# Optimization experiments

Hardware: AMD Instinct MI355X
Metric: run time of the kernel (lower is better)

## Reference

```python
import jax, jax.numpy as jnp
import numpy as np
from jax import lax

# Module config (mirrors init_kwargs)
N, CIN, COUT, H, W = 16, 512, 512, 64, 64
KS = 3          # conv kernel_size
FACTOR = 2
GAIN = 1.0
LRMUL = 1.0
FIR_1D = np.array([1.0, 3.0, 3.0, 1.0], dtype=np.float32)

# upfirdn pad amounts as in the torch code
FIRN = 4
P = FIRN - FACTOR + (KS - 1)      # = 4
PAD0 = (P + 1) // 2               # = 2
PAD1 = P // 2                     # = 2
W_LRMUL = GAIN / np.sqrt(CIN * COUT * KS * KS)  # he_std * lrmul (use_wscale)
B_LRMUL = LRMUL
SQRT2 = np.float32(np.sqrt(2.0))


def setup_inputs() -> dict:
    key = jax.random.key(0)
    kx, kw, kb = jax.random.split(key, 3)
    x = jax.random.normal(kx, (N, CIN, H, W), dtype=jnp.float32)
    # weight init: randn * init_std, init_std = 1/lrmul = 1.0 under use_wscale
    weight = jax.random.normal(kw, (COUT, CIN, KS, KS), dtype=jnp.float32)
    bias = jax.random.normal(kb, (COUT,), dtype=jnp.float32) * 0.1
    kf = np.outer(FIR_1D, FIR_1D)
    kf = kf / kf.sum() * GAIN
    fir = jnp.asarray(kf, dtype=jnp.float32)  # [4,4], non-trainable
    return {"x": x, "weight": weight, "bias": bias, "fir": fir}


def _blur_and_resize(x, fir):
    # x: [N, C, H, W]; FIR blur via depthwise trick: fold C into batch.
    n, c, h, w = x.shape
    y = x.reshape(n * c, 1, h, w)
    y = jnp.pad(y, ((0, 0), (0, 0), (PAD0, PAD1), (PAD0, PAD1)))
    # valid conv with 4x4 FIR -> [n*c, 1, h+1, w+1]
    y = lax.conv_general_dilated(
        y, fir[None, None, :, :], window_strides=(1, 1), padding="VALID",
        dimension_numbers=("NCHW", "OIHW", "NCHW"))
    # F.interpolate(mode='nearest') from (h+1, w+1) back to (h, w):
    # torch nearest uses src = floor(dst * in/out) == (dst*(h+1))//h
    ri = (jnp.arange(h) * (h + 1)) // h
    ci = (jnp.arange(w) * (w + 1)) // w
    y = y[:, :, ri, :][:, :, :, ci]
    return y.reshape(n, c, h, w)


def reference(x, weight, bias, fir):
    y = _blur_and_resize(x, fir)
    # strided conv: stride=factor, padding=ks//2 (SAME-ish), cross-correlation
    out = lax.conv_general_dilated(
        y, weight * W_LRMUL, window_strides=(FACTOR, FACTOR),
        padding=[(KS // 2, KS // 2), (KS // 2, KS // 2)],
        dimension_numbers=("NCHW", "OIHW", "NCHW"))
    out = out + (bias * B_LRMUL)[None, :, None, None]
    out = jnp.where(out >= 0, out, 0.2 * out) * SQRT2  # leaky_relu(0.2) * sqrt(2)
    return out
```

## Files before the change

### kernel.cpp

```cpp
#include <hip/hip_runtime.h>
#include <hip/hip_bf16.h>
#include <stdint.h>

#define N_IMG 16
#define C_IN  512
#define C_OUT 512
#define H_IN  64
#define W_IN  64
#define OH    32
#define OW    32
#define PIX   (N_IMG*OH*OW)

#define YPH 65
#define YPW 33

#define W2_ELEMS (9*C_OUT*C_IN)
#define W2_BYTES (W2_ELEMS*2)

typedef __attribute__((ext_vector_type(8))) __bf16 bf16x8;
typedef __attribute__((ext_vector_type(4))) float  f32x4;

__device__ inline void gload_lds16(const void* g, void* l) {
  __builtin_amdgcn_global_load_lds(
      (const __attribute__((address_space(1))) void*)g,
      (__attribute__((address_space(3))) void*)l, 16, 0, 0);
}

__global__ __launch_bounds__(256) void prep_w_kernel(const float* __restrict__ w,
                                                     __hip_bfloat16* __restrict__ w2) {
  int id = blockIdx.x * 256 + threadIdx.x;
  const float* p = w + (size_t)id * 9;
  float v[9];
#pragma unroll
  for (int t = 0; t < 9; ++t) v[t] = p[t] * (1.0f/1536.0f);
#pragma unroll
  for (int t = 0; t < 9; ++t)
    w2[(size_t)t*(C_OUT*C_IN) + id] = __float2bfloat16(v[t]);
}

__global__ __launch_bounds__(256) void blur_kernel(const float* __restrict__ x,
                                                   __hip_bfloat16* __restrict__ yt) {
  __shared__ float obuf[2][32][65];
  const int tid = threadIdx.x;
  const int c   = tid >> 3;
  const int p8  = tid & 7;
  const int w8  = p8 * 8;
  const int r0  = blockIdx.x * 8;
  const int cib = blockIdx.y;
  const int n   = blockIdx.z;
  const float* xc = x + ((size_t)(n*C_IN + cib*32 + c) * H_IN) * W_IN + w8;

  {
    const uint4 z4 = {0u, 0u, 0u, 0u};
    if (tid < 16) {
      int hh  = r0 + (tid >> 1);
      int par = tid & 1;
      size_t slot = (((size_t)n*YPH + hh + 1)*2 + par)*YPW;
      uint4* p = (uint4*)(yt + slot*C_IN + cib*32);
      p[0]=z4; p[1]=z4; p[2]=z4; p[3]=z4;
    }
    if (blockIdx.x == 0 && tid < 66) {
      int par = tid / 33;
      int cc  = tid - par*33;
      size_t slot = ((size_t)n*YPH*2 + par)*YPW + cc;
      uint4* p = (uint4*)(yt + slot*C_IN + cib*32);
      p[0]=z4; p[1]=z4; p[2]=z4; p[3]=z4;
    }
  }

  const int rp_oc  = tid & 3;
  const int rp_p   = tid >> 2;
  const int rp_par = rp_p & 1;
  const int rp_ch  = rp_p >> 1;

  float cur[8], nxt[8];
  float h1[8], h2[8], h3[8];
#pragma unroll
  for (int j = 0; j < 8; ++j) { h1[j] = 0.f; h2[j] = 0.f; h3[j] = 0.f; }

  auto load_row = [&](int r, float* dst) {
    if (r >= 0 && r < H_IN) {
      const float4 a = *(const float4*)(xc + (size_t)r * W_IN);
      const float4 b = *(const float4*)(xc + (size_t)r * W_IN + 4);
      dst[0]=a.x; dst[1]=a.y; dst[2]=a.z; dst[3]=a.w;
      dst[4]=b.x; dst[5]=b.y; dst[6]=b.z; dst[7]=b.w;
    } else {
#pragma unroll
      for (int j = 0; j < 8; ++j) dst[j] = 0.f;
    }
  };

  load_row(r0 - 2, cur);
  for (int ri = 0; ri < 11; ++ri) {
    const int r = r0 - 2 + ri;
    if (ri < 10) load_row(r + 1, nxt);

    float l2 = __shfl_up(cur[6], 1);
    float l1 = __shfl_up(cur[7], 1);
    float rr = __shfl_down(cur[0], 1);
    if (p8 == 0) { l2 = 0.f; l1 = 0.f; }
    if (p8 == 7) { rr = 0.f; }
    float hc[8];
    hc[0] = l2 + 3.f*(l1 + cur[0]) + cur[1];
    hc[1] = l1 + 3.f*(cur[0] + cur[1]) + cur[2];
#pragma unroll
    for (int j = 2; j < 7; ++j) hc[j] = cur[j-2] + 3.f*(cur[j-1] + cur[j]) + cur[j+1];
    hc[7] = cur[5] + 3.f*(cur[6] + cur[7]) + rr;

    if (ri >= 3) {
      const int h = r - 1;
      const int b = ri & 1;
#pragma unroll
      for (int j = 0; j < 8; ++j)
        obuf[b][c][w8 + j] = (h3[j] + 3.f*(h2[j] + h1[j]) + hc[j]) * (1.0f/64.0f);
      __syncthreads();
      alignas(16) __hip_bfloat16 t16[8];
#pragma unroll
      for (int j = 0; j < 8; ++j)
        t16[j] = __float2bfloat16(obuf[b][rp_oc*8 + j][rp_p]);
      size_t slot = ((size_t)(n*YPH + h + 1)*2 + rp_par)*YPW + rp_ch + 1;
      *(uint4*)(yt + slot*C_IN + cib*32 + rp_oc*8) = *(uint4*)t16;
    }

#pragma unroll
    for (int j = 0; j < 8; ++j) {
      h3[j] = h2[j]; h2[j] = h1[j]; h1[j] = hc[j]; cur[j] = nxt[j];
    }
  }
}

#define ABYTES (128*64*2)
__global__ __launch_bounds__(256, 2) void conv_kernel(const __hip_bfloat16* __restrict__ w2,
                            const __hip_bfloat16* __restrict__ yt,
                            const float* __restrict__ bias,
                            float* __restrict__ out) {
  __shared__ __hip_bfloat16 Alds[2][128*64];
  __shared__ __hip_bfloat16 Blds[2][128*64];
  const int tid  = threadIdx.x;
  const int lane = tid & 63;
  const int wv   = tid >> 6;
  const int wm   = wv & 1;
  const int wn   = wv >> 1;
  const int cob0 = blockIdx.y * 128;
  const int pixb = blockIdx.x * 128;
  const int quad = lane >> 4;
  const int wvb  = tid & 192;

  size_t aoff[4];
  int    bseg8[4], bn65[4], boh2[4], bow_[4];
  int    ldsOff[4];
#pragma unroll
  for (int i = 0; i < 4; ++i) {
    int s = i*256 + tid;
    int r = s >> 3;
    int pp = s & 7;
    int gg = pp ^ (r & 7);
    aoff[i] = (size_t)(cob0 + r)*C_IN + gg*8;
    int gp = pixb + r;
    bn65[i] = (gp >> 10) * YPH;
    boh2[i] = ((gp >> 5) & 31) * 2;
    bow_[i] = gp & 31;
    bseg8[i] = gg*8;
    ldsOff[i] = (i*256 + wvb)*16;
  }

  auto stage = [&](int c, int b) {
    const int t   = c >> 3;
    const int cib = (c & 7) << 6;
    const int kh  = (t * 11) >> 5;
    const int kw  = t - kh*3;
    const int par = (kw == 1) ? 0 : 1;
    const int d   = (kw == 0) ? 0 : 1;
    const __hip_bfloat16* wt = w2 + (size_t)t * (C_OUT*C_IN) + cib;
#pragma unroll
    for (int i = 0; i < 4; ++i)
      gload_lds16(wt + aoff[i], (char*)Alds + b*ABYTES + ldsOff[i]);
#pragma unroll
    for (int i = 0; i < 4; ++i) {
      size_t slot = ((size_t)(bn65[i] + boh2[i] + kh)*2 + par)*YPW + bow_[i] + d;
      gload_lds16(yt + slot*C_IN + bseg8[i] + cib, (char*)Blds + b*ABYTES + ldsOff[i]);
    }
  };

  f32x4 acc[4][4];
  const f32x4 zero = {0.f, 0.f, 0.f, 0.f};
#pragma unroll
  for (int mi = 0; mi < 4; ++mi)
#pragma unroll
    for (int ni = 0; ni < 4; ++ni) acc[mi][ni] = zero;

  stage(0, 0);
#pragma unroll 2
  for (int cch = 0; cch < 72; ++cch) {
    __syncthreads();
    if (cch < 71) stage(cch + 1, (cch + 1) & 1);
    const int b = cch & 1;
    const char* Ab = (const char*)Alds + b*ABYTES;
    const char* Bb = (const char*)Blds + b*ABYTES;
#pragma unroll
    for (int kk = 0; kk < 2; ++kk) {
      bf16x8 af[4], bfr[4];
#pragma unroll
      for (int mi = 0; mi < 4; ++mi) {
        int r = wm*64 + mi*16 + (lane & 15);
        int gsg = kk*4 + quad;
        af[mi] = *(const bf16x8*)(Ab + r*128 + ((gsg ^ (r & 7))*16));
      }
#pragma unroll
      for (int ni = 0; ni < 4; ++ni) {
        int r = wn*64 + ni*16 + (lane & 15);
        int gsg = kk*4 + quad;
        bfr[ni] = *(const bf16x8*)(Bb + r*128 + ((gsg ^ (r & 7))*16));
      }
#pragma unroll
      for (int mi = 0; mi < 4; ++mi)
#pragma unroll
        for (int ni = 0; ni < 4; ++ni)
          acc[mi][ni] = __builtin_amdgcn_mfma_f32_16x16x32_bf16(af[mi], bfr[ni], acc[mi][ni], 0, 0, 0);
    }
  }

#pragma unroll
  for (int mi = 0; mi < 4; ++mi) {
#pragma unroll
    for (int reg = 0; reg < 4; ++reg) {
      int co = cob0 + wm*64 + mi*16 + quad*4 + reg;
      float bv = bias[co];
#pragma unroll
      for (int ni = 0; ni < 4; ++ni) {
        int gp  = pixb + wn*64 + ni*16 + (lane & 15);
        int n   = gp >> 10;
        int ohw = gp & 1023;
        float v = acc[mi][ni][reg] + bv;
        v = (v >= 0.f ? v : 0.2f*v) * 1.41421356f;
        out[(((size_t)n*C_OUT + co) << 10) + ohw] = v;
      }
    }
  }
}

extern "C" void kernel_launch(void* const* d_in, const int* in_sizes, int n_in,
                              void* d_out, int out_size, void* d_ws, size_t ws_size,
                              hipStream_t stream) {
  const float* x    = (const float*)d_in[0];
  const float* w    = (const float*)d_in[1];
  const float* bias = (const float*)d_in[2];
  float* out = (float*)d_out;
  __hip_bfloat16* w2 = (__hip_bfloat16*)d_ws;
  __hip_bfloat16* yt = (__hip_bfloat16*)((char*)d_ws + W2_BYTES);

  prep_w_kernel<<<(C_OUT*C_IN)/256, 256, 0, stream>>>(w, w2);
  blur_kernel<<<dim3(8, 16, 16), 256, 0, stream>>>(x, yt);
  conv_kernel<<<dim3(PIX/128, C_OUT/128), 256, 0, stream>>>(w2, yt, bias, out);
}
```

Baseline: 307.6 us.

## Load weight fragments directly from global into registers, drop A LDS staging

The weight (A) operand is no longer staged through shared memory. Each lane now loads its own MFMA fragments straight from global memory into a double-buffered register array, prefetched one K-chunk ahead. This halves LDS traffic and footprint and removes the LDS reads for A. In exchange it adds register pressure (32 extra VGPRs of prefetch), and the global loads are not coalesced across waves; two waves sharing wm fetch the same rows redundantly.

```diff
diff --git a/kernel.cpp b/kernel.cpp
--- a/kernel.cpp
+++ b/kernel.cpp
@@ -129,12 +129,11 @@
   }
 }
 
-#define ABYTES (128*64*2)
+#define BBYTES (128*64*2)
 __global__ __launch_bounds__(256, 2) void conv_kernel(const __hip_bfloat16* __restrict__ w2,
                             const __hip_bfloat16* __restrict__ yt,
                             const float* __restrict__ bias,
                             float* __restrict__ out) {
-  __shared__ __hip_bfloat16 Alds[2][128*64];
   __shared__ __hip_bfloat16 Blds[2][128*64];
   const int tid  = threadIdx.x;
   const int lane = tid & 63;
@@ -146,16 +145,12 @@
   const int quad = lane >> 4;
   const int wvb  = tid & 192;
 
-  size_t aoff[4];
-  int    bseg8[4], bn65[4], boh2[4], bow_[4];
-  int    ldsOff[4];
+  int bseg8[4], bn65[4], boh2[4], bow_[4], ldsOff[4];
 #pragma unroll
   for (int i = 0; i < 4; ++i) {
     int s = i*256 + tid;
     int r = s >> 3;
-    int pp = s & 7;
-    int gg = pp ^ (r & 7);
-    aoff[i] = (size_t)(cob0 + r)*C_IN + gg*8;
+    int gg = (s & 7) ^ (r & 7);
     int gp = pixb + r;
     bn65[i] = (gp >> 10) * YPH;
     boh2[i] = ((gp >> 5) & 31) * 2;
@@ -164,22 +159,35 @@
     ldsOff[i] = (i*256 + wvb)*16;
   }
 
-  auto stage = [&](int c, int b) {
+  size_t aRow[4];
+#pragma unroll
+  for (int mi = 0; mi < 4; ++mi)
+    aRow[mi] = (size_t)(cob0 + wm*64 + mi*16 + (lane & 15))*C_IN + quad*8;
+
+  auto stageB = [&](int c, int b) {
     const int t   = c >> 3;
     const int cib = (c & 7) << 6;
     const int kh  = (t * 11) >> 5;
     const int kw  = t - kh*3;
     const int par = (kw == 1) ? 0 : 1;
     const int d   = (kw == 0) ? 0 : 1;
-    const __hip_bfloat16* wt = w2 + (size_t)t * (C_OUT*C_IN) + cib;
-#pragma unroll
-    for (int i = 0; i < 4; ++i)
-      gload_lds16(wt + aoff[i], (char*)Alds + b*ABYTES + ldsOff[i]);
 #pragma unroll
     for (int i = 0; i < 4; ++i) {
       size_t slot = ((size_t)(bn65[i] + boh2[i] + kh)*2 + par)*YPW + bow_[i] + d;
-      gload_lds16(yt + slot*C_IN + bseg8[i] + cib, (char*)Blds + b*ABYTES + ldsOff[i]);
-    }
+      gload_lds16(yt + slot*C_IN + bseg8[i] + cib, (char*)Blds + b*BBYTES + ldsOff[i]);
+    }
+  };
+
+  bf16x8 afb[2][4][2];
+  auto loadA = [&](int c, int b) {
+    const int t   = c >> 3;
+    const int cib = (c & 7) << 6;
+    const __hip_bfloat16* base = w2 + (size_t)t*(C_OUT*C_IN) + cib;
+#pragma unroll
+    for (int mi = 0; mi < 4; ++mi)
+#pragma unroll
+      for (int kk = 0; kk < 2; ++kk)
+        afb[b][mi][kk] = *(const bf16x8*)(base + aRow[mi] + kk*32);
   };
 
   f32x4 acc[4][4];
@@ -189,23 +197,20 @@
 #pragma unroll
     for (int ni = 0; ni < 4; ++ni) acc[mi][ni] = zero;
 
-  stage(0, 0);
+  stageB(0, 0);
+  loadA(0, 0);
 #pragma unroll 2
   for (int cch = 0; cch < 72; ++cch) {
     __syncthreads();
-    if (cch < 71) stage(cch + 1, (cch + 1) & 1);
+    if (cch < 71) {
+      stageB(cch + 1, (cch + 1) & 1);
+      loadA(cch + 1, (cch + 1) & 1);
+    }
     const int b = cch & 1;
-    const char* Ab = (const char*)Alds + b*ABYTES;
-    const char* Bb = (const char*)Blds + b*ABYTES;
+    const char* Bb = (const char*)Blds + b*BBYTES;
 #pragma unroll
     for (int kk = 0; kk < 2; ++kk) {
-      bf16x8 af[4], bfr[4];
-#pragma unroll
-      for (int mi = 0; mi < 4; ++mi) {
-        int r = wm*64 + mi*16 + (lane & 15);
-        int gsg = kk*4 + quad;
-        af[mi] = *(const bf16x8*)(Ab + r*128 + ((gsg ^ (r & 7))*16));
-      }
+      bf16x8 bfr[4];
 #pragma unroll
       for (int ni = 0; ni < 4; ++ni) {
         int r = wn*64 + ni*16 + (lane & 15);
@@ -216,7 +221,7 @@
       for (int mi = 0; mi < 4; ++mi)
 #pragma unroll
         for (int ni = 0; ni < 4; ++ni)
-          acc[mi][ni] = __builtin_amdgcn_mfma_f32_16x16x32_bf16(af[mi], bfr[ni], acc[mi][ni], 0, 0, 0);
+          acc[mi][ni] = __builtin_amdgcn_mfma_f32_16x16x32_bf16(afb[b][mi][kk], bfr[ni], acc[mi][ni], 0, 0, 0);
     }
   }
 
```

New measurement: 691.1 us. +124.7%, slower.
